# Kernel optimization log

Measured on AMD Instinct MI355X. Metric: run time of the kernel, lower is better.

Reference implementation:

```python
import jax, jax.numpy as jnp
import numpy as np


def _gcn(x, src, dst, W, b, M):
    # GCNConv: out = D^{-1/2} (A+I) D^{-1/2} X W + b, messages flow src->dst
    xw = x @ W  # [M, D]
    loops = jnp.arange(M)
    s = jnp.concatenate([src, loops])
    d = jnp.concatenate([dst, loops])
    deg = jax.ops.segment_sum(jnp.ones_like(s, x.dtype), d, num_segments=M)
    dinv = jnp.where(deg > 0, jax.lax.rsqrt(jnp.maximum(deg, 1.0)), 0.0)
    norm = dinv[s] * dinv[d]  # [Eg+M]
    return jax.ops.segment_sum(norm[:, None] * xw[s], d, num_segments=M) + b


def _graph_cross_attention(values, k, q, e_src, e_dst, N):
    # gather-dot, segment softmax over destination tokens, scatter-sum of values
    scale = jnp.sqrt(jnp.asarray(k.shape[1], k.dtype))
    dots = (q[e_dst] * k[e_src]).sum(-1) / scale  # [Ea]
    m = jax.ops.segment_max(dots, e_dst, num_segments=N)
    m = jnp.where(jnp.isfinite(m), m, 0.0)
    w = jnp.exp(dots - m[e_dst])
    den = jax.ops.segment_sum(w, e_dst, num_segments=N)
    w = w / jnp.where(den > 0, den, 1.0)[e_dst]
    return jax.ops.segment_sum(w[:, None] * values[e_src], e_dst, num_segments=N)


def reference(token_embeddings, tokens2edges, edge_index, e2t_src, e2t_dst,
              W_gnn, b_gnn, Wk, bk, Wq, bq, Wl, bl, gate_a, gate_b):
    N = token_embeddings.shape[1]
    M = tokens2edges.shape[1]

    def per_sample(t, t2e, ei, es, ed):
        edge_emb = t[t2e]                                  # [M, D] gather
        edge_emb = _gcn(edge_emb, ei[0], ei[1], W_gnn, b_gnn, M)
        k = edge_emb @ Wk + bk                             # [M, 64]
        q = t @ Wq + bq                                    # [N, 64]
        gatt = _graph_cross_attention(edge_emb, k, q, es, ed, N)  # [N, D]
        new = t + jnp.tanh(gate_a) * gatt
        new = new + jnp.tanh(gate_b) * (new @ Wl + bl)
        return new

    return jax.vmap(per_sample)(token_embeddings, tokens2edges, edge_index, e2t_src, e2t_dst)


def setup_inputs() -> dict:
    B, N, M, Eg, Ea, D, DK = 4, 4096, 16384, 65536, 65536, 512, 64
    key = jax.random.key(0)
    ks = jax.random.split(key, 16)
    s = 0.05  # weight scale to keep activations well-conditioned
    return {
        "token_embeddings": jax.random.normal(ks[0], (B, N, D), jnp.float32),
        "tokens2edges": jax.random.randint(ks[1], (B, M), 0, N),
        "edge_index": jax.random.randint(ks[2], (B, 2, Eg), 0, M),
        "e2t_src": jax.random.randint(ks[3], (B, Ea), 0, M),
        "e2t_dst": jax.random.randint(ks[4], (B, Ea), 0, N),
        "W_gnn": jax.random.normal(ks[5], (D, D), jnp.float32) * s,
        "b_gnn": jax.random.normal(ks[6], (D,), jnp.float32) * s,
        "Wk": jax.random.normal(ks[7], (D, DK), jnp.float32) * s,
        "bk": jax.random.normal(ks[8], (DK,), jnp.float32) * s,
        "Wq": jax.random.normal(ks[9], (D, DK), jnp.float32) * s,
        "bq": jax.random.normal(ks[10], (DK,), jnp.float32) * s,
        "Wl": jax.random.normal(ks[11], (D, D), jnp.float32) * s,
        "bl": jax.random.normal(ks[12], (D,), jnp.float32) * s,
        "gate_a": jax.random.normal(ks[13], (1,), jnp.float32),
        "gate_b": jax.random.normal(ks[14], (1,), jnp.float32),
    }
```

## Files before the change

### kernel.cpp

```cpp
#include <hip/hip_runtime.h>
#include <math.h>

#define BB 4
#define NT 4096
#define ME 16384
#define EG 65536
#define EA 65536
#define DD 512
#define DKK 64

using bf16x8 = __attribute__((ext_vector_type(8))) short;
using f32x4  = __attribute__((ext_vector_type(4))) float;

static __device__ __forceinline__ unsigned short f2bf(float f) {
    unsigned u = __float_as_uint(f);
    u += 0x7fffu + ((u >> 16) & 1u);
    return (unsigned short)(u >> 16);
}
static __device__ __forceinline__ float bf2f(unsigned short u) {
    return __uint_as_float((unsigned)u << 16);
}
static __device__ __forceinline__ void acc8(float* a, uint4 v, float s) {
    a[0] += s * __uint_as_float(v.x << 16);
    a[1] += s * __uint_as_float(v.x & 0xffff0000u);
    a[2] += s * __uint_as_float(v.y << 16);
    a[3] += s * __uint_as_float(v.y & 0xffff0000u);
    a[4] += s * __uint_as_float(v.z << 16);
    a[5] += s * __uint_as_float(v.z & 0xffff0000u);
    a[6] += s * __uint_as_float(v.w << 16);
    a[7] += s * __uint_as_float(v.w & 0xffff0000u);
}
static __device__ __forceinline__ uint4 pack8(const float* a) {
    uint4 o;
    o.x = (unsigned)f2bf(a[0]) | ((unsigned)f2bf(a[1]) << 16);
    o.y = (unsigned)f2bf(a[2]) | ((unsigned)f2bf(a[3]) << 16);
    o.z = (unsigned)f2bf(a[4]) | ((unsigned)f2bf(a[5]) << 16);
    o.w = (unsigned)f2bf(a[6]) | ((unsigned)f2bf(a[7]) << 16);
    return o;
}

__global__ void k_hist2(const int* __restrict__ ei_all, const int* __restrict__ ed_all,
                        int* __restrict__ cntG, int* __restrict__ cntA) {
    int i = blockIdx.x * 256 + threadIdx.x;
    if (i < BB * EG) {
        int b = i >> 16, e = i & (EG - 1);
        int dst = ei_all[(size_t)b * 2 * EG + EG + e];
        atomicAdd(&cntG[b * ME + dst], 1);
    } else {
        int j = i - BB * EG;
        atomicAdd(&cntA[(j >> 16) * NT + ed_all[j]], 1);
    }
}

__global__ __launch_bounds__(1024) void k_scan2(
    const int* __restrict__ cntG, int* __restrict__ offsG, int* __restrict__ curG,
    float* __restrict__ dinv,
    const int* __restrict__ cntA, int* __restrict__ offsA, int* __restrict__ curA) {
    __shared__ int sums[1024];
    int tid = threadIdx.x;
    int bid = blockIdx.x;
    const int* cnt;
    int *offs, *cur;
    float* dv = nullptr;
    int C, nk;
    if (bid < BB) {
        cnt = cntG + bid * ME; offs = offsG + bid * (ME + 1); cur = curG + bid * ME;
        dv = dinv + bid * ME; C = ME / 1024; nk = ME;
    } else {
        int b = bid - BB;
        cnt = cntA + b * NT; offs = offsA + b * (NT + 1); cur = curA + b * NT;
        C = NT / 1024; nk = NT;
    }
    int local[16];
    int tot = 0;
    for (int i = 0; i < C; ++i) { local[i] = cnt[tid * C + i]; tot += local[i]; }
    sums[tid] = tot;
    __syncthreads();
    for (int d = 1; d < 1024; d <<= 1) {
        int v = (tid >= d) ? sums[tid - d] : 0;
        __syncthreads();
        sums[tid] += v;
        __syncthreads();
    }
    int run = sums[tid] - tot;
    for (int i = 0; i < C; ++i) {
        int idx = tid * C + i;
        offs[idx] = run;
        cur[idx] = run;
        if (dv) dv[idx] = rsqrtf((float)local[i] + 1.0f);
        run += local[i];
    }
    if (tid == 1023) offs[nk] = run;
}

__global__ void k_fill2(const int* __restrict__ ei_all, const int* __restrict__ es_all,
                        const int* __restrict__ ed_all, const int* __restrict__ t2e_all,
                        const float* __restrict__ dinv,
                        int* __restrict__ curG, int2* __restrict__ csrG,
                        int* __restrict__ curA, int2* __restrict__ csrA) {
    int i = blockIdx.x * 256 + threadIdx.x;
    if (i < BB * EG) {
        int b = i >> 16, e = i & (EG - 1);
        const int* ei = ei_all + (size_t)b * 2 * EG;
        int s = ei[e], d = ei[EG + e];
        int p = atomicAdd(&curG[b * ME + d], 1);
        int2 v;
        v.x = t2e_all[(b << 14) + s];
        v.y = __float_as_int(dinv[b * ME + s]);
        csrG[(size_t)b * EG + p] = v;
    } else {
        int j = i - BB * EG;
        int b = j >> 16;
        int p = atomicAdd(&curA[b * NT + ed_all[j]], 1);
        int2 v;
        v.x = es_all[j];
        v.y = ed_all[j];
        csrA[(size_t)b * EA + p] = v;
    }
}

__global__ void k_cast(const float* __restrict__ x, unsigned short* __restrict__ xb) {
    long i = (long)blockIdx.x * blockDim.x + threadIdx.x;
    float4 v = *(const float4*)(x + (i << 2));
    ushort4 o;
    o.x = f2bf(v.x); o.y = f2bf(v.y); o.z = f2bf(v.z); o.w = f2bf(v.w);
    *(ushort4*)(xb + (i << 2)) = o;
}

__global__ void k_wtT(const float* __restrict__ Wgnn, const float* __restrict__ Wk,
                      const float* __restrict__ Wq, const float* __restrict__ Wl,
                      unsigned short* __restrict__ BtT, unsigned short* __restrict__ Wlt) {
    int i = blockIdx.x * 256 + threadIdx.x;
    if (i < 640 * 512) {
        int n = i >> 9, k = i & 511;
        float v;
        if (n < 512)      v = Wgnn[((long)k << 9) + n];
        else if (n < 576) {
            int c = n - 512;
            const float* wr = Wgnn + ((long)k << 9);
            float s = 0.0f;
            for (int j = 0; j < DD; ++j) s += wr[j] * Wk[j * 64 + c];
            v = s;
        } else            v = Wq[k * 64 + (n - 576)];
        BtT[i] = f2bf(v);
    } else {
        int j = i - 640 * 512;
        int n = j >> 9, k = j & 511;
        Wlt[j] = f2bf(Wl[((long)k << 9) + n]);
    }
}

__global__ __launch_bounds__(256) void k_bias(
    const float* __restrict__ bgnn, const float* __restrict__ Wk,
    const float* __restrict__ bk, const float* __restrict__ bq,
    float* __restrict__ biasG, float* __restrict__ bias640) {
    int bx = blockIdx.x, tid = threadIdx.x;
    if (bx < 3) {
        int i = bx * 256 + tid;
        if (i < 512) { biasG[i] = bgnn[i]; bias640[i] = 0.0f; }
        else if (i < 576) { bias640[i] = 0.0f; }
        else if (i < 640) { bias640[i] = bq[i - 576]; }
        return;
    }
    int n = bx - 3;
    __shared__ float red[256];
    float s = 0.0f;
    for (int k = tid; k < DD; k += 256) s += bgnn[k] * Wk[k * 64 + n];
    red[tid] = s;
    __syncthreads();
    for (int d = 128; d > 0; d >>= 1) {
        if (tid < d) red[tid] += red[tid + d];
        __syncthreads();
    }
    if (tid == 0) biasG[512 + n] = red[0] + bk[n];
}

__global__ __launch_bounds__(256, 2) void gemm_token(
    const unsigned short* __restrict__ A, const unsigned short* __restrict__ BtT,
    const float* __restrict__ bias640, unsigned short* __restrict__ Xg,
    unsigned short* __restrict__ Xk, unsigned short* __restrict__ qmatb)
{
    __shared__ short As[64 * 32];
    __shared__ short Bs[320 * 32];
    int tid = threadIdx.x;
    int lane = tid & 63;
    int w = tid >> 6;
    long bm = (long)blockIdx.x * 64;
    int bcol = blockIdx.y * 320;
    const unsigned short* Bblk = BtT + (long)bcol * DD;

    f32x4 acc[4][5] = {};

    for (int k0 = 0; k0 < DD; k0 += 32) {
        {
            int s = tid;
            int r = s >> 2;
            int gc = ((s & 3) ^ ((s >> 3) & 3)) * 8;
            __builtin_amdgcn_global_load_lds(
                (const __attribute__((address_space(1))) unsigned int*)(A + (bm + r) * DD + k0 + gc),
                (__attribute__((address_space(3))) unsigned int*)(As + s * 8), 16, 0, 0);
        }
#pragma unroll
        for (int i = 0; i < 5; ++i) {
            int s = tid + i * 256;
            int r = s >> 2;
            int gc = ((s & 3) ^ ((s >> 3) & 3)) * 8;
            __builtin_amdgcn_global_load_lds(
                (const __attribute__((address_space(1))) unsigned int*)(Bblk + (long)r * DD + k0 + gc),
                (__attribute__((address_space(3))) unsigned int*)(Bs + s * 8), 16, 0, 0);
        }
        __syncthreads();

        int cq = lane >> 4;
        bf16x8 af[4];
#pragma unroll
        for (int rb = 0; rb < 4; ++rb) {
            int r = rb * 16 + (lane & 15);
            af[rb] = *(const bf16x8*)&As[(r * 4 + (cq ^ ((r >> 1) & 3))) * 8];
        }
#pragma unroll
        for (int cb = 0; cb < 5; ++cb) {
            int r = w * 80 + cb * 16 + (lane & 15);
            bf16x8 bf = *(const bf16x8*)&Bs[(r * 4 + (cq ^ ((r >> 1) & 3))) * 8];
#pragma unroll
            for (int rb = 0; rb < 4; ++rb)
                acc[rb][cb] = __builtin_amdgcn_mfma_f32_16x16x32_bf16(af[rb], bf, acc[rb][cb], 0, 0, 0);
        }
        __syncthreads();
    }

#pragma unroll
    for (int rb = 0; rb < 4; ++rb) {
        long row0 = bm + rb * 16 + ((lane >> 4) << 2);
#pragma unroll
        for (int cb = 0; cb < 5; ++cb) {
            int col = bcol + w * 80 + cb * 16 + (lane & 15);
            float bv = bias640[col];
            if (col < 512) {
#pragma unroll
                for (int r = 0; r < 4; ++r)
                    Xg[(row0 + r) * DD + col] = f2bf(acc[rb][cb][r] + bv);
            } else if (col < 576) {
#pragma unroll
                for (int r = 0; r < 4; ++r)
                    Xk[(row0 + r) * DKK + (col - 512)] = f2bf(acc[rb][cb][r] + bv);
            } else {
#pragma unroll
                for (int r = 0; r < 4; ++r)
                    qmatb[(row0 + r) * DKK + (col - 576)] = f2bf(acc[rb][cb][r] + bv);
            }
        }
    }
}

__global__ __launch_bounds__(256) void k_gcn_gather(
    const unsigned short* __restrict__ Xg, const unsigned short* __restrict__ Xk,
    const int* __restrict__ t2e_all, const float* __restrict__ dinv,
    const int* __restrict__ offsG, const int2* __restrict__ csrG,
    const float* __restrict__ biasG,
    unsigned short* __restrict__ eeb, unsigned short* __restrict__ kmatb)
{
    int w = threadIdx.x >> 6;
    int lane = threadIdx.x & 63;
    int bx = blockIdx.x;
    int b = (bx & 7) >> 1;
    int half = bx & 1;
    int idx = bx >> 3;
    int m = (half * 2048 + idx) * 4 + w;
    int mg = (b << 14) + m;
    const int* offs = offsG + b * (ME + 1);
    const int2* csr = csrG + (size_t)b * EG;
    const unsigned short* gl = Xg + (((long)b * NT) << 9) + lane * 8;
    const unsigned short* kl = Xk + ((long)b * NT) * DKK + lane;

    float dm = dinv[mg];
    int self = t2e_all[mg];
    uint4 vself = *(const uint4*)(gl + ((long)self << 9));
    float kself = bf2f(kl[(long)self * DKK]);

    float a[8] = {0, 0, 0, 0, 0, 0, 0, 0};
    float ak = 0.0f;
    int p = offs[m], end = offs[m + 1];
    for (; p + 4 <= end; p += 4) {
        int2 e0 = csr[p], e1 = csr[p + 1], e2 = csr[p + 2], e3 = csr[p + 3];
        uint4 r0 = *(const uint4*)(gl + ((long)e0.x << 9));
        uint4 r1 = *(const uint4*)(gl + ((long)e1.x << 9));
        uint4 r2 = *(const uint4*)(gl + ((long)e2.x << 9));
        uint4 r3 = *(const uint4*)(gl + ((long)e3.x << 9));
        float k0 = bf2f(kl[(long)e0.x * DKK]);
        float k1 = bf2f(kl[(long)e1.x * DKK]);
        float k2 = bf2f(kl[(long)e2.x * DKK]);
        float k3 = bf2f(kl[(long)e3.x * DKK]);
        float w0 = __int_as_float(e0.y), w1 = __int_as_float(e1.y);
        float w2 = __int_as_float(e2.y), w3 = __int_as_float(e3.y);
        acc8(a, r0, w0); ak += w0 * k0;
        acc8(a, r1, w1); ak += w1 * k1;
        acc8(a, r2, w2); ak += w2 * k2;
        acc8(a, r3, w3); ak += w3 * k3;
    }
    if (p < end) {
        int e1m = end - 1;
        int i1 = min(p + 1, e1m), i2 = min(p + 2, e1m), i3 = min(p + 3, e1m);
        int2 e0 = csr[p], e1 = csr[i1], e2 = csr[i2], e3 = csr[i3];
        uint4 r0 = *(const uint4*)(gl + ((long)e0.x << 9));
        uint4 r1 = *(const uint4*)(gl + ((long)e1.x << 9));
        uint4 r2 = *(const uint4*)(gl + ((long)e2.x << 9));
        uint4 r3 = *(const uint4*)(gl + ((long)e3.x << 9));
        float k0 = bf2f(kl[(long)e0.x * DKK]);
        float k1 = bf2f(kl[(long)e1.x * DKK]);
        float k2 = bf2f(kl[(long)e2.x * DKK]);
        float k3 = bf2f(kl[(long)e3.x * DKK]);
        float w0 = __int_as_float(e0.y);
        float w1 = (p + 1 < end) ? __int_as_float(e1.y) : 0.0f;
        float w2 = (p + 2 < end) ? __int_as_float(e2.y) : 0.0f;
        float w3 = (p + 3 < end) ? __int_as_float(e3.y) : 0.0f;
        acc8(a, r0, w0); ak += w0 * k0;
        acc8(a, r1, w1); ak += w1 * k1;
        acc8(a, r2, w2); ak += w2 * k2;
        acc8(a, r3, w3); ak += w3 * k3;
    }
    acc8(a, vself, dm);
    ak += dm * kself;

    const float* bg = biasG + lane * 8;
    float4 b0 = *(const float4*)bg;
    float4 b1 = *(const float4*)(bg + 4);
    a[0] = dm * a[0] + b0.x; a[1] = dm * a[1] + b0.y;
    a[2] = dm * a[2] + b0.z; a[3] = dm * a[3] + b0.w;
    a[4] = dm * a[4] + b1.x; a[5] = dm * a[5] + b1.y;
    a[6] = dm * a[6] + b1.z; a[7] = dm * a[7] + b1.w;
    *(uint4*)(eeb + ((long)mg << 9) + lane * 8) = pack8(a);
    kmatb[(long)mg * DKK + lane] = f2bf(dm * ak + biasG[512 + lane]);
}

__global__ void k_dots(const unsigned short* __restrict__ kmatb,
                       const unsigned short* __restrict__ qmatb,
                       const int2* __restrict__ csrA, int2* __restrict__ swbuf) {
    int bx = blockIdx.x;
    int b = (bx & 7) >> 1;
    int half = bx & 1;
    int idx = bx >> 3;
    int p = (b << 16) + (half * 128 + idx) * 256 + threadIdx.x;
    int2 sd = csrA[p];
    const uint4* kr = (const uint4*)(kmatb + ((long)(b * ME + sd.x) << 6));
    const uint4* qr = (const uint4*)(qmatb + ((long)(b * NT + sd.y) << 6));
    float dot = 0.0f;
#pragma unroll
    for (int j = 0; j < 8; ++j) {
        uint4 kv = kr[j];
        uint4 qv = qr[j];
        dot += __uint_as_float(kv.x << 16) * __uint_as_float(qv.x << 16)
             + __uint_as_float(kv.x & 0xffff0000u) * __uint_as_float(qv.x & 0xffff0000u)
             + __uint_as_float(kv.y << 16) * __uint_as_float(qv.y << 16)
             + __uint_as_float(kv.y & 0xffff0000u) * __uint_as_float(qv.y & 0xffff0000u)
             + __uint_as_float(kv.z << 16) * __uint_as_float(qv.z << 16)
             + __uint_as_float(kv.z & 0xffff0000u) * __uint_as_float(qv.z & 0xffff0000u)
             + __uint_as_float(kv.w << 16) * __uint_as_float(qv.w << 16)
             + __uint_as_float(kv.w & 0xffff0000u) * __uint_as_float(qv.w & 0xffff0000u);
    }
    int2 o;
    o.x = sd.x;
    o.y = __float_as_int(expf(dot * 0.125f));
    swbuf[p] = o;
}

__global__ __launch_bounds__(256) void k_att_gather(
    const unsigned short* __restrict__ eeb, const int2* __restrict__ swbuf,
    const int* __restrict__ offsA,
    const float* __restrict__ t_all, const float* __restrict__ ga,
    float* __restrict__ out, unsigned short* __restrict__ nb)
{
    int ng = (blockIdx.x * 256 + threadIdx.x) >> 6;
    int lane = threadIdx.x & 63;
    int b = ng >> 12;
    int n = ng & (NT - 1);
    const int* offs = offsA + b * (NT + 1);
    const int2* swb = swbuf + (size_t)b * EA;
    const unsigned short* el = eeb + (((size_t)b * ME) << 9) + lane * 8;

    float a[8] = {0, 0, 0, 0, 0, 0, 0, 0};
    float den = 0.0f;
    int p = offs[n], end = offs[n + 1];
    for (; p + 8 <= end; p += 8) {
        int2 e0 = swb[p],     e1 = swb[p + 1], e2 = swb[p + 2], e3 = swb[p + 3];
        int2 e4 = swb[p + 4], e5 = swb[p + 5], e6 = swb[p + 6], e7 = swb[p + 7];
        uint4 r0 = *(const uint4*)(el + ((long)e0.x << 9));
        uint4 r1 = *(const uint4*)(el + ((long)e1.x << 9));
        uint4 r2 = *(const uint4*)(el + ((long)e2.x << 9));
        uint4 r3 = *(const uint4*)(el + ((long)e3.x << 9));
        uint4 r4 = *(const uint4*)(el + ((long)e4.x << 9));
        uint4 r5 = *(const uint4*)(el + ((long)e5.x << 9));
        uint4 r6 = *(const uint4*)(el + ((long)e6.x << 9));
        uint4 r7 = *(const uint4*)(el + ((long)e7.x << 9));
        float w0 = __int_as_float(e0.y), w1 = __int_as_float(e1.y);
        float w2 = __int_as_float(e2.y), w3 = __int_as_float(e3.y);
        float w4 = __int_as_float(e4.y), w5 = __int_as_float(e5.y);
        float w6 = __int_as_float(e6.y), w7 = __int_as_float(e7.y);
        den += (w0 + w1 + w2 + w3) + (w4 + w5 + w6 + w7);
        acc8(a, r0, w0);
        acc8(a, r1, w1);
        acc8(a, r2, w2);
        acc8(a, r3, w3);
        acc8(a, r4, w4);
        acc8(a, r5, w5);
        acc8(a, r6, w6);
        acc8(a, r7, w7);
    }
    if (p < end) {
        int e1m = end - 1;
        int2 e0 = swb[p];
        int2 e1 = swb[min(p + 1, e1m)];
        int2 e2 = swb[min(p + 2, e1m)];
        int2 e3 = swb[min(p + 3, e1m)];
        int2 e4 = swb[min(p + 4, e1m)];
        int2 e5 = swb[min(p + 5, e1m)];
        int2 e6 = swb[min(p + 6, e1m)];
        int2 e7 = swb[min(p + 7, e1m)];
        uint4 r0 = *(const uint4*)(el + ((long)e0.x << 9));
        uint4 r1 = *(const uint4*)(el + ((long)e1.x << 9));
        uint4 r2 = *(const uint4*)(el + ((long)e2.x << 9));
        uint4 r3 = *(const uint4*)(el + ((long)e3.x << 9));
        uint4 r4 = *(const uint4*)(el + ((long)e4.x << 9));
        uint4 r5 = *(const uint4*)(el + ((long)e5.x << 9));
        uint4 r6 = *(const uint4*)(el + ((long)e6.x << 9));
        uint4 r7 = *(const uint4*)(el + ((long)e7.x << 9));
        float w0 = __int_as_float(e0.y);
        float w1 = (p + 1 < end) ? __int_as_float(e1.y) : 0.0f;
        float w2 = (p + 2 < end) ? __int_as_float(e2.y) : 0.0f;
        float w3 = (p + 3 < end) ? __int_as_float(e3.y) : 0.0f;
        float w4 = (p + 4 < end) ? __int_as_float(e4.y) : 0.0f;
        float w5 = (p + 5 < end) ? __int_as_float(e5.y) : 0.0f;
        float w6 = (p + 6 < end) ? __int_as_float(e6.y) : 0.0f;
        float w7 = (p + 7 < end) ? __int_as_float(e7.y) : 0.0f;
        den += (w0 + w1 + w2 + w3) + (w4 + w5 + w6 + w7);
        acc8(a, r0, w0);
        acc8(a, r1, w1);
        acc8(a, r2, w2);
        acc8(a, r3, w3);
        acc8(a, r4, w4);
        acc8(a, r5, w5);
        acc8(a, r6, w6);
        acc8(a, r7, w7);
    }
    float g = tanhf(ga[0]);
    float inv = den > 0.0f ? g / den : 0.0f;
    const float* tr = t_all + ((long)ng << 9) + lane * 8;
    float4 t0 = *(const float4*)tr;
    float4 t1 = *(const float4*)(tr + 4);
    float o[8];
    o[0] = t0.x + inv * a[0]; o[1] = t0.y + inv * a[1];
    o[2] = t0.z + inv * a[2]; o[3] = t0.w + inv * a[3];
    o[4] = t1.x + inv * a[4]; o[5] = t1.y + inv * a[5];
    o[6] = t1.z + inv * a[6]; o[7] = t1.w + inv * a[7];
    float* op = out + ((long)ng << 9) + lane * 8;
    *(float4*)op = make_float4(o[0], o[1], o[2], o[3]);
    *(float4*)(op + 4) = make_float4(o[4], o[5], o[6], o[7]);
    *(uint4*)(nb + ((long)ng << 9) + lane * 8) = pack8(o);
}

__global__ __launch_bounds__(256, 2) void gemm_final(
    const unsigned short* __restrict__ A, const unsigned short* __restrict__ Bt,
    const float* __restrict__ bias, float* __restrict__ Cf, const float* __restrict__ gs)
{
    constexpr int CB = 8;
    constexpr int BROWS = 2 * CB * 16;
    __shared__ short As[128 * 32];
    __shared__ short Bs[BROWS * 32];
    int tid = threadIdx.x;
    int lane = tid & 63;
    int w = tid >> 6;
    int wm = w >> 1, wn = w & 1;
    long bm = (long)blockIdx.x * 128;
    int bcol = blockIdx.y * BROWS;
    const unsigned short* Bblk = Bt + (long)bcol * DD;

    f32x4 acc[4][CB] = {};

    for (int k0 = 0; k0 < DD; k0 += 32) {
#pragma unroll
        for (int i = 0; i < 2; ++i) {
            int s = tid + i * 256;
            int r = s >> 2;
            int gc = ((s & 3) ^ ((s >> 3) & 3)) * 8;
            __builtin_amdgcn_global_load_lds(
                (const __attribute__((address_space(1))) unsigned int*)(A + (bm + r) * DD + k0 + gc),
                (__attribute__((address_space(3))) unsigned int*)(As + s * 8), 16, 0, 0);
        }
#pragma unroll
        for (int i = 0; i < CB / 2; ++i) {
            int s = tid + i * 256;
            int r = s >> 2;
            int gc = ((s & 3) ^ ((s >> 3) & 3)) * 8;
            __builtin_amdgcn_global_load_lds(
                (const __attribute__((address_space(1))) unsigned int*)(Bblk + (long)r * DD + k0 + gc),
                (__attribute__((address_space(3))) unsigned int*)(Bs + s * 8), 16, 0, 0);
        }
        __syncthreads();

        int cq = lane >> 4;
        bf16x8 af[4];
#pragma unroll
        for (int rb = 0; rb < 4; ++rb) {
            int r = wm * 64 + rb * 16 + (lane & 15);
            af[rb] = *(const bf16x8*)&As[(r * 4 + (cq ^ ((r >> 1) & 3))) * 8];
        }
#pragma unroll
        for (int cb = 0; cb < CB; ++cb) {
            int r = wn * (CB * 16) + cb * 16 + (lane & 15);
            bf16x8 bf = *(const bf16x8*)&Bs[(r * 4 + (cq ^ ((r >> 1) & 3))) * 8];
#pragma unroll
            for (int rb = 0; rb < 4; ++rb)
                acc[rb][cb] = __builtin_amdgcn_mfma_f32_16x16x32_bf16(af[rb], bf, acc[rb][cb], 0, 0, 0);
        }
        __syncthreads();
    }

    float g = tanhf(gs[0]);
#pragma unroll
    for (int rb = 0; rb < 4; ++rb) {
        long row0 = bm + wm * 64 + rb * 16 + ((lane >> 4) << 2);
#pragma unroll
        for (int cb = 0; cb < CB; ++cb) {
            int col = bcol + wn * (CB * 16) + cb * 16 + (lane & 15);
            float bv = bias[col];
#pragma unroll
            for (int r = 0; r < 4; ++r)
                Cf[(row0 + r) * DD + col] += g * (acc[rb][cb][r] + bv);
        }
    }
}

extern "C" void kernel_launch(void* const* d_in, const int* in_sizes, int n_in,
                              void* d_out, int out_size, void* d_ws, size_t ws_size,
                              hipStream_t stream) {
    const float* t_all   = (const float*)d_in[0];
    const int*   t2e_all = (const int*)d_in[1];
    const int*   ei_all  = (const int*)d_in[2];
    const int*   es_all  = (const int*)d_in[3];
    const int*   ed_all  = (const int*)d_in[4];
    const float* Wgnn    = (const float*)d_in[5];
    const float* bgnn    = (const float*)d_in[6];
    const float* Wk      = (const float*)d_in[7];
    const float* bk      = (const float*)d_in[8];
    const float* Wq      = (const float*)d_in[9];
    const float* bq      = (const float*)d_in[10];
    const float* Wl      = (const float*)d_in[11];
    const float* bl      = (const float*)d_in[12];
    const float* ga      = (const float*)d_in[13];
    const float* gb      = (const float*)d_in[14];
    float* out = (float*)d_out;

    char* wsb = (char*)d_ws;
    size_t off = 0;
    unsigned short* eeb   = (unsigned short*)(wsb + off); off += (size_t)BB * ME * DD * 2;
    unsigned short* tb    = (unsigned short*)(wsb + off); off += (size_t)BB * NT * DD * 2;
    unsigned short* Xg    = (unsigned short*)(wsb + off); off += (size_t)BB * NT * DD * 2;
    unsigned short* nb    = (unsigned short*)(wsb + off); off += (size_t)BB * NT * DD * 2;
    unsigned short* Xk    = (unsigned short*)(wsb + off); off += (size_t)BB * NT * DKK * 2;
    unsigned short* qmatb = (unsigned short*)(wsb + off); off += (size_t)BB * NT * DKK * 2;
    unsigned short* kmatb = (unsigned short*)(wsb + off); off += (size_t)BB * ME * DKK * 2;
    unsigned short* BtT   = (unsigned short*)(wsb + off); off += (size_t)640 * DD * 2;
    unsigned short* Wlt   = (unsigned short*)(wsb + off); off += (size_t)DD * DD * 2;
    float* biasG   = (float*)(wsb + off); off += 576 * 4;
    float* bias640 = (float*)(wsb + off); off += 640 * 4;
    float* dinv  = (float*)(wsb + off); off += (size_t)BB * ME * 4;
    int2* swbuf  = (int2*)(wsb + off); off += (size_t)BB * EA * 8;
    int* cntG  = (int*)(wsb + off); off += (size_t)BB * ME * 4;
    int* cntA  = (int*)(wsb + off); off += (size_t)BB * NT * 4;
    int* offsG = (int*)(wsb + off); off += (size_t)BB * (ME + 1) * 4;
    int* curG  = (int*)(wsb + off); off += (size_t)BB * ME * 4;
    int2* csrG = (int2*)(wsb + off); off += (size_t)BB * EG * 8;
    int* offsA = (int*)(wsb + off); off += (size_t)BB * (NT + 1) * 4;
    int* curA  = (int*)(wsb + off); off += (size_t)BB * NT * 4;
    int2* csrA = (int2*)(wsb + off); off += (size_t)BB * EA * 8;

    k_wtT<<<(1152 * DD) / 256, 256, 0, stream>>>(Wgnn, Wk, Wq, Wl, BtT, Wlt);
    k_bias<<<67, 256, 0, stream>>>(bgnn, Wk, bk, bq, biasG, bias640);

    hipMemsetAsync(cntG, 0, (size_t)BB * (ME + NT) * 4, stream);
    k_hist2<<<(BB * (EG + EA)) / 256, 256, 0, stream>>>(ei_all, ed_all, cntG, cntA);
    k_scan2<<<2 * BB, 1024, 0, stream>>>(cntG, offsG, curG, dinv, cntA, offsA, curA);
    k_fill2<<<(BB * (EG + EA)) / 256, 256, 0, stream>>>(
        ei_all, es_all, ed_all, t2e_all, dinv, curG, csrG, curA, csrA);

    k_cast<<<(int)(((long)BB * NT * DD / 4) / 256), 256, 0, stream>>>(t_all, tb);
    gemm_token<<<dim3((BB * NT) / 64, 2), 256, 0, stream>>>(tb, BtT, bias640, Xg, Xk, qmatb);

    k_gcn_gather<<<(BB * ME * 64) / 256, 256, 0, stream>>>(
        Xg, Xk, t2e_all, dinv, offsG, csrG, biasG, eeb, kmatb);

    k_dots<<<(BB * EA) / 256, 256, 0, stream>>>(kmatb, qmatb, csrA, swbuf);
    k_att_gather<<<(BB * NT * 64) / 256, 256, 0, stream>>>(
        eeb, swbuf, offsA, t_all, ga, out, nb);

    gemm_final<<<dim3((BB * NT) / 128, 2), 256, 0, stream>>>(nb, Wlt, bl, out, gb);
}
```

Measured before the change: 361.0 us.

## Merge prep kernels and fuse CSR fill with token GEMM launch

Merges the weight transpose, bias, cast and histogram kernels into one launch with block-range dispatch. The CSR fill work now runs as extra blocks inside the token GEMM kernel, so the two overlap instead of running serially. The attention gather also gets a new block-to-node mapping that spreads batches and halves across consecutive blocks. This cuts launch overhead and idle gaps, but fill blocks inherit the GEMM's launch bounds and shared-memory allocation, which could lower their occupancy.

```diff
diff --git a/kernel.cpp b/kernel.cpp
--- a/kernel.cpp
+++ b/kernel.cpp
@@ -39,16 +39,76 @@
     return o;
 }
 
-__global__ void k_hist2(const int* __restrict__ ei_all, const int* __restrict__ ed_all,
-                        int* __restrict__ cntG, int* __restrict__ cntA) {
-    int i = blockIdx.x * 256 + threadIdx.x;
-    if (i < BB * EG) {
-        int b = i >> 16, e = i & (EG - 1);
-        int dst = ei_all[(size_t)b * 2 * EG + EG + e];
-        atomicAdd(&cntG[b * ME + dst], 1);
+#define PREP_WTT   2304
+#define PREP_BIAS  (PREP_WTT + 67)
+#define PREP_CAST  (PREP_BIAS + 8192)
+#define PREP_HIST  (PREP_CAST + 2048)
+__global__ __launch_bounds__(256) void k_prep(
+    const float* __restrict__ Wgnn, const float* __restrict__ Wk,
+    const float* __restrict__ Wq, const float* __restrict__ Wl,
+    const float* __restrict__ bgnn, const float* __restrict__ bk,
+    const float* __restrict__ bq, const float* __restrict__ t_all,
+    const int* __restrict__ ei_all, const int* __restrict__ ed_all,
+    unsigned short* __restrict__ BtT, unsigned short* __restrict__ Wlt,
+    float* __restrict__ biasG, float* __restrict__ bias640,
+    unsigned short* __restrict__ tb, int* __restrict__ cntG, int* __restrict__ cntA)
+{
+    __shared__ float red[256];
+    int bx = blockIdx.x, tid = threadIdx.x;
+    if (bx < PREP_WTT) {
+        int i = bx * 256 + tid;
+        if (i < 640 * 512) {
+            int n = i >> 9, k = i & 511;
+            float v;
+            if (n < 512)      v = Wgnn[((long)k << 9) + n];
+            else if (n < 576) {
+                int c = n - 512;
+                const float* wr = Wgnn + ((long)k << 9);
+                float s = 0.0f;
+                for (int j = 0; j < DD; ++j) s += wr[j] * Wk[j * 64 + c];
+                v = s;
+            } else            v = Wq[k * 64 + (n - 576)];
+            BtT[i] = f2bf(v);
+        } else {
+            int j = i - 640 * 512;
+            int n = j >> 9, k = j & 511;
+            Wlt[j] = f2bf(Wl[((long)k << 9) + n]);
+        }
+    } else if (bx < PREP_BIAS) {
+        int bb = bx - PREP_WTT;
+        if (bb < 3) {
+            int i = bb * 256 + tid;
+            if (i < 512) { biasG[i] = bgnn[i]; bias640[i] = 0.0f; }
+            else if (i < 576) { bias640[i] = 0.0f; }
+            else if (i < 640) { bias640[i] = bq[i - 576]; }
+            return;
+        }
+        int n = bb - 3;
+        float s = 0.0f;
+        for (int k = tid; k < DD; k += 256) s += bgnn[k] * Wk[k * 64 + n];
+        red[tid] = s;
+        __syncthreads();
+        for (int d = 128; d > 0; d >>= 1) {
+            if (tid < d) red[tid] += red[tid + d];
+            __syncthreads();
+        }
+        if (tid == 0) biasG[512 + n] = red[0] + bk[n];
+    } else if (bx < PREP_CAST) {
+        long i = (long)(bx - PREP_BIAS) * 256 + tid;
+        float4 v = *(const float4*)(t_all + (i << 2));
+        ushort4 o;
+        o.x = f2bf(v.x); o.y = f2bf(v.y); o.z = f2bf(v.z); o.w = f2bf(v.w);
+        *(ushort4*)(tb + (i << 2)) = o;
     } else {
-        int j = i - BB * EG;
-        atomicAdd(&cntA[(j >> 16) * NT + ed_all[j]], 1);
+        int i = (bx - PREP_CAST) * 256 + tid;
+        if (i < BB * EG) {
+            int b = i >> 16, e = i & (EG - 1);
+            int dst = ei_all[(size_t)b * 2 * EG + EG + e];
+            atomicAdd(&cntG[b * ME + dst], 1);
+        } else {
+            int j = i - BB * EG;
+            atomicAdd(&cntA[(j >> 16) * NT + ed_all[j]], 1);
+        }
     }
 }
 
@@ -93,89 +153,12 @@
     if (tid == 1023) offs[nk] = run;
 }
 
-__global__ void k_fill2(const int* __restrict__ ei_all, const int* __restrict__ es_all,
-                        const int* __restrict__ ed_all, const int* __restrict__ t2e_all,
-                        const float* __restrict__ dinv,
-                        int* __restrict__ curG, int2* __restrict__ csrG,
-                        int* __restrict__ curA, int2* __restrict__ csrA) {
-    int i = blockIdx.x * 256 + threadIdx.x;
-    if (i < BB * EG) {
-        int b = i >> 16, e = i & (EG - 1);
-        const int* ei = ei_all + (size_t)b * 2 * EG;
-        int s = ei[e], d = ei[EG + e];
-        int p = atomicAdd(&curG[b * ME + d], 1);
-        int2 v;
-        v.x = t2e_all[(b << 14) + s];
-        v.y = __float_as_int(dinv[b * ME + s]);
-        csrG[(size_t)b * EG + p] = v;
-    } else {
-        int j = i - BB * EG;
-        int b = j >> 16;
-        int p = atomicAdd(&curA[b * NT + ed_all[j]], 1);
-        int2 v;
-        v.x = es_all[j];
-        v.y = ed_all[j];
-        csrA[(size_t)b * EA + p] = v;
-    }
-}
-
-__global__ void k_cast(const float* __restrict__ x, unsigned short* __restrict__ xb) {
-    long i = (long)blockIdx.x * blockDim.x + threadIdx.x;
-    float4 v = *(const float4*)(x + (i << 2));
-    ushort4 o;
-    o.x = f2bf(v.x); o.y = f2bf(v.y); o.z = f2bf(v.z); o.w = f2bf(v.w);
-    *(ushort4*)(xb + (i << 2)) = o;
-}
-
-__global__ void k_wtT(const float* __restrict__ Wgnn, const float* __restrict__ Wk,
-                      const float* __restrict__ Wq, const float* __restrict__ Wl,
-                      unsigned short* __restrict__ BtT, unsigned short* __restrict__ Wlt) {
-    int i = blockIdx.x * 256 + threadIdx.x;
-    if (i < 640 * 512) {
-        int n = i >> 9, k = i & 511;
-        float v;
-        if (n < 512)      v = Wgnn[((long)k << 9) + n];
-        else if (n < 576) {
-            int c = n - 512;
-            const float* wr = Wgnn + ((long)k << 9);
-            float s = 0.0f;
-            for (int j = 0; j < DD; ++j) s += wr[j] * Wk[j * 64 + c];
-            v = s;
-        } else            v = Wq[k * 64 + (n - 576)];
-        BtT[i] = f2bf(v);
-    } else {
-        int j = i - 640 * 512;
-        int n = j >> 9, k = j & 511;
-        Wlt[j] = f2bf(Wl[((long)k << 9) + n]);
-    }
-}
-
-__global__ __launch_bounds__(256) void k_bias(
-    const float* __restrict__ bgnn, const float* __restrict__ Wk,
-    const float* __restrict__ bk, const float* __restrict__ bq,
-    float* __restrict__ biasG, float* __restrict__ bias640) {
-    int bx = blockIdx.x, tid = threadIdx.x;
-    if (bx < 3) {
-        int i = bx * 256 + tid;
-        if (i < 512) { biasG[i] = bgnn[i]; bias640[i] = 0.0f; }
-        else if (i < 576) { bias640[i] = 0.0f; }
-        else if (i < 640) { bias640[i] = bq[i - 576]; }
-        return;
-    }
-    int n = bx - 3;
-    __shared__ float red[256];
-    float s = 0.0f;
-    for (int k = tid; k < DD; k += 256) s += bgnn[k] * Wk[k * 64 + n];
-    red[tid] = s;
-    __syncthreads();
-    for (int d = 128; d > 0; d >>= 1) {
-        if (tid < d) red[tid] += red[tid + d];
-        __syncthreads();
-    }
-    if (tid == 0) biasG[512 + n] = red[0] + bk[n];
-}
-
-__global__ __launch_bounds__(256, 2) void gemm_token(
+__global__ __launch_bounds__(256, 2) void k_fill_token(
+    const int* __restrict__ ei_all, const int* __restrict__ es_all,
+    const int* __restrict__ ed_all, const int* __restrict__ t2e_all,
+    const float* __restrict__ dinv,
+    int* __restrict__ curG, int2* __restrict__ csrG,
+    int* __restrict__ curA, int2* __restrict__ csrA,
     const unsigned short* __restrict__ A, const unsigned short* __restrict__ BtT,
     const float* __restrict__ bias640, unsigned short* __restrict__ Xg,
     unsigned short* __restrict__ Xk, unsigned short* __restrict__ qmatb)
@@ -183,10 +166,35 @@
     __shared__ short As[64 * 32];
     __shared__ short Bs[320 * 32];
     int tid = threadIdx.x;
+    int bxx = blockIdx.x;
+
+    if (bxx >= 512) {
+        int i = (bxx - 512) * 256 + tid;
+        if (i < BB * EG) {
+            int b = i >> 16, e = i & (EG - 1);
+            const int* ei = ei_all + (size_t)b * 2 * EG;
+            int s = ei[e], d = ei[EG + e];
+            int p = atomicAdd(&curG[b * ME + d], 1);
+            int2 v;
+            v.x = t2e_all[(b << 14) + s];
+            v.y = __float_as_int(dinv[b * ME + s]);
+            csrG[(size_t)b * EG + p] = v;
+        } else {
+            int j = i - BB * EG;
+            int b = j >> 16;
+            int p = atomicAdd(&curA[b * NT + ed_all[j]], 1);
+            int2 v;
+            v.x = es_all[j];
+            v.y = ed_all[j];
+            csrA[(size_t)b * EA + p] = v;
+        }
+        return;
+    }
+
     int lane = tid & 63;
     int w = tid >> 6;
-    long bm = (long)blockIdx.x * 64;
-    int bcol = blockIdx.y * 320;
+    long bm = (long)(bxx >> 1) * 64;
+    int bcol = (bxx & 1) * 320;
     const unsigned short* Bblk = BtT + (long)bcol * DD;
 
     f32x4 acc[4][5] = {};
@@ -370,10 +378,14 @@
     const float* __restrict__ t_all, const float* __restrict__ ga,
     float* __restrict__ out, unsigned short* __restrict__ nb)
 {
-    int ng = (blockIdx.x * 256 + threadIdx.x) >> 6;
+    int w = threadIdx.x >> 6;
     int lane = threadIdx.x & 63;
-    int b = ng >> 12;
-    int n = ng & (NT - 1);
+    int bx = blockIdx.x;
+    int b = (bx & 7) >> 1;
+    int half = bx & 1;
+    int idx = bx >> 3;
+    int n = (half * 512 + idx) * 4 + w;
+    int ng = (b << 12) + n;
     const int* offs = offsA + b * (NT + 1);
     const int2* swb = swbuf + (size_t)b * EA;
     const unsigned short* el = eeb + (((size_t)b * ME) << 9) + lane * 8;
@@ -574,17 +586,16 @@
     int* curA  = (int*)(wsb + off); off += (size_t)BB * NT * 4;
     int2* csrA = (int2*)(wsb + off); off += (size_t)BB * EA * 8;
 
-    k_wtT<<<(1152 * DD) / 256, 256, 0, stream>>>(Wgnn, Wk, Wq, Wl, BtT, Wlt);
-    k_bias<<<67, 256, 0, stream>>>(bgnn, Wk, bk, bq, biasG, bias640);
-
     hipMemsetAsync(cntG, 0, (size_t)BB * (ME + NT) * 4, stream);
-    k_hist2<<<(BB * (EG + EA)) / 256, 256, 0, stream>>>(ei_all, ed_all, cntG, cntA);
+    k_prep<<<PREP_HIST, 256, 0, stream>>>(
+        Wgnn, Wk, Wq, Wl, bgnn, bk, bq, t_all, ei_all, ed_all,
+        BtT, Wlt, biasG, bias640, tb, cntG, cntA);
+
     k_scan2<<<2 * BB, 1024, 0, stream>>>(cntG, offsG, curG, dinv, cntA, offsA, curA);
-    k_fill2<<<(BB * (EG + EA)) / 256, 256, 0, stream>>>(
-        ei_all, es_all, ed_all, t2e_all, dinv, curG, csrG, curA, csrA);
-
-    k_cast<<<(int)(((long)BB * NT * DD / 4) / 256), 256, 0, stream>>>(t_all, tb);
-    gemm_token<<<dim3((BB * NT) / 64, 2), 256, 0, stream>>>(tb, BtT, bias640, Xg, Xk, qmatb);
+
+    k_fill_token<<<512 + 2048, 256, 0, stream>>>(
+        ei_all, es_all, ed_all, t2e_all, dinv, curG, csrG, curA, csrA,
+        tb, BtT, bias640, Xg, Xk, qmatb);
 
     k_gcn_gather<<<(BB * ME * 64) / 256, 256, 0, stream>>>(
         Xg, Xk, t2e_all, dinv, offsG, csrG, biasG, eeb, kmatb);
```

Measured after the change: 334.7 us. -7.3%, faster.
